# Kernel optimization log

Hardware: AMD Instinct MI355X
Metric: run time of the kernel (lower is better)

The kernel has to match this reference:

```python
import jax, jax.numpy as jnp
import numpy as np
import math

GOLDEN_CENTER = 1.0 / math.e
GOLDEN_LOWER = 0.5 - math.log(4.0 / 3.0)
GOLDEN_UPPER = 0.5

B, T, D = 4, 2048, 1024
E = 8
I = 4096 // (E // 2)  # expert_inter = 1024


def setup_inputs() -> dict:
    key = jax.random.key(0)
    k = jax.random.split(key, 6)
    s_d = 1.0 / math.sqrt(D)
    s_i = 1.0 / math.sqrt(I)
    return {
        "x": jax.random.normal(k[0], (B, T, D), jnp.float32),
        "Wg": jax.random.normal(k[1], (E, D, I), jnp.float32) * s_d,
        "Wu": jax.random.normal(k[2], (E, D, I), jnp.float32) * s_d,
        "Wd": jax.random.normal(k[3], (E, I, D), jnp.float32) * s_i,
        "Wr": jax.random.normal(k[4], (D, E), jnp.float32) * s_d,
        "temperature": jnp.ones((1,), jnp.float32),
    }


def _routing_weights(x, Wr, temperature):
    # inhibition: [B,T,E]
    inh = jax.nn.sigmoid((x @ Wr) / temperature)
    in_zone = (inh >= GOLDEN_LOWER) & (inh <= GOLDEN_UPPER)
    dist = jnp.abs(inh - GOLDEN_CENTER)
    w = jnp.exp(-dist / 0.1) * in_zone.astype(x.dtype)
    wsum = w.sum(axis=-1, keepdims=True)
    no_expert = wsum < 1e-8
    # fallback: softer decay, keep top-2 experts, renormalize
    fb = jnp.exp(-dist / 0.3)
    _, top2 = jax.lax.top_k(fb, 2)  # [B,T,2]
    fb_mask = jax.nn.one_hot(top2, E, dtype=x.dtype).sum(axis=-2)  # [B,T,E]
    fb_w = fb * fb_mask
    fb_w = fb_w / jnp.clip(fb_w.sum(axis=-1, keepdims=True), 1e-8)
    w = jnp.where(no_expert, fb_w, w)
    wsum = w.sum(axis=-1, keepdims=True)
    return w / jnp.clip(wsum, 1e-8)


def reference(x, Wg, Wu, Wd, Wr, temperature):
    weights = _routing_weights(x, Wr, temperature)  # [B,T,E]
    gate = jnp.einsum("btd,edi->beti", x, Wg)
    up = jnp.einsum("btd,edi->beti", x, Wu)
    h = jax.nn.silu(gate) * up  # [B,E,T,I]
    e_out = jnp.einsum("beti,eid->betd", h, Wd)
    out = jnp.einsum("bte,betd->btd", weights, e_out)
    return out
```

## Files before the change

kernel.cpp:

```cpp
#include <hip/hip_runtime.h>
#include <hip/hip_bf16.h>
#include <cstdint>

typedef __attribute__((ext_vector_type(8))) _Float16 f16x8;
typedef __attribute__((ext_vector_type(4))) _Float16 f16x4;
typedef __attribute__((ext_vector_type(4))) float f32x4;

#define GOLDEN_CENTER_F 0.36787944117144233f
#define GOLDEN_LOWER_F  0.21231792754821915f
#define GOLDEN_UPPER_F  0.5f

static constexpr int Dm = 1024;
static constexpr int Im = 1024;
static constexpr int NTOK = 8192;
static constexpr int NE = 8;

__device__ __forceinline__ void async16(const _Float16* g, _Float16* l) {
  __builtin_amdgcn_global_load_lds(
      (const __attribute__((address_space(1))) void*)g,
      (__attribute__((address_space(3))) void*)l,
      16, 0, 0);
}

__global__ void routing_kernel(const float* __restrict__ x, const float* __restrict__ Wr,
                               const float* __restrict__ temp, float* __restrict__ wts) {
  const int wave = threadIdx.x >> 6, lane = threadIdx.x & 63;
  const int t = blockIdx.x * 4 + wave;
  const float* xr = x + (size_t)t * Dm;
  float acc[NE] = {0.f,0.f,0.f,0.f,0.f,0.f,0.f,0.f};
  for (int d = lane; d < Dm; d += 64) {
    float xv = xr[d];
    const float* wr = Wr + (size_t)d * NE;
#pragma unroll
    for (int e = 0; e < NE; ++e) acc[e] += xv * wr[e];
  }
#pragma unroll
  for (int off = 32; off > 0; off >>= 1) {
#pragma unroll
    for (int e = 0; e < NE; ++e) acc[e] += __shfl_down(acc[e], off, 64);
  }
  if (lane == 0) {
    float T = temp[0];
    float w[NE], dist[NE];
    float wsum = 0.f;
#pragma unroll
    for (int e = 0; e < NE; ++e) {
      float inh = 1.f / (1.f + expf(-acc[e] / T));
      dist[e] = fabsf(inh - GOLDEN_CENTER_F);
      bool zone = (inh >= GOLDEN_LOWER_F) && (inh <= GOLDEN_UPPER_F);
      w[e] = zone ? expf(-dist[e] / 0.1f) : 0.f;
      wsum += w[e];
    }
    if (wsum < 1e-8f) {
      float fb[NE];
#pragma unroll
      for (int e = 0; e < NE; ++e) fb[e] = expf(-dist[e] / 0.3f);
      int i1 = 0;
      for (int e = 1; e < NE; ++e) if (fb[e] > fb[i1]) i1 = e;
      int i2 = (i1 == 0) ? 1 : 0;
      for (int e = 0; e < NE; ++e) if (e != i1 && fb[e] > fb[i2]) i2 = e;
      float s = fmaxf(fb[i1] + fb[i2], 1e-8f);
#pragma unroll
      for (int e = 0; e < NE; ++e) w[e] = 0.f;
      w[i1] = fb[i1] / s;
      w[i2] = fb[i2] / s;
      wsum = w[i1] + w[i2];
    }
    float inv = 1.f / fmaxf(wsum, 1e-8f);
#pragma unroll
    for (int e = 0; e < NE; ++e) wts[(size_t)t * NE + e] = w[e] * inv;
  }
}

__global__ void compact_kernel(const float* __restrict__ wts, int* __restrict__ tok,
                               float* __restrict__ wc, int* __restrict__ cnt,
                               int* __restrict__ pos) {
  const int e = blockIdx.x;
  const int tid = threadIdx.x;
  const int wave = tid >> 6, lane = tid & 63;
  __shared__ int wcnt[4];
  __shared__ int s_running;
  if (tid == 0) s_running = 0;
  __syncthreads();
  for (int base = 0; base < NTOK; base += 256) {
    int t = base + tid;
    float w = wts[(size_t)t * NE + e];
    bool act = w > 0.f;
    unsigned long long mask = __ballot(act);
    int prefix = __popcll(mask & ((1ull << lane) - 1ull));
    if (lane == 0) wcnt[wave] = __popcll(mask);
    __syncthreads();
    int wbase = 0;
    for (int i = 0; i < wave; ++i) wbase += wcnt[i];
    int run = s_running;
    int p = run + wbase + prefix;
    pos[(size_t)t * NE + e] = act ? p : -1;
    if (act) {
      tok[(size_t)e * NTOK + p] = t;
      wc[(size_t)e * NTOK + p] = w;
    }
    __syncthreads();
    if (tid == 0) s_running = run + wcnt[0] + wcnt[1] + wcnt[2] + wcnt[3];
    __syncthreads();
  }
  int c = s_running;
  if (tid == 0) cnt[e] = c;
  int padded = (c + 127) & ~127;
  for (int p = c + tid; p < padded; p += 256) {
    tok[(size_t)e * NTOK + p] = 0;
    wc[(size_t)e * NTOK + p] = 0.f;
  }
}

__global__ void cvt_x_kernel(const float* __restrict__ x, _Float16* __restrict__ xb) {
  size_t i = ((size_t)blockIdx.x * 256 + threadIdx.x) * 4;
  float4 v = *(const float4*)(x + i);
  f16x4 o = {(_Float16)v.x, (_Float16)v.y, (_Float16)v.z, (_Float16)v.w};
  *(f16x4*)(xb + i) = o;
}

__global__ void transpose_cvt_kernel(const float* __restrict__ Wg, const float* __restrict__ Wu,
                                     const float* __restrict__ Wd, _Float16* __restrict__ WgT,
                                     _Float16* __restrict__ WuT, _Float16* __restrict__ WdT) {
  __shared__ float tile[32][33];
  const int which = blockIdx.z >> 3;
  const int e = blockIdx.z & 7;
  const float* src = which == 0 ? Wg : which == 1 ? Wu : Wd;
  _Float16* dst = which == 0 ? WgT : which == 1 ? WuT : WdT;
  const size_t base = (size_t)e * 1024 * 1024;
  const int r0 = blockIdx.y * 32, c0 = blockIdx.x * 32;
  const int tx = threadIdx.x & 31, ty = threadIdx.x >> 5;
#pragma unroll
  for (int j = 0; j < 32; j += 8)
    tile[ty + j][tx] = src[base + (size_t)(r0 + ty + j) * 1024 + c0 + tx];
  __syncthreads();
#pragma unroll
  for (int j = 0; j < 32; j += 8)
    dst[base + (size_t)(c0 + ty + j) * 1024 + r0 + tx] = (_Float16)tile[tx][ty + j];
}

__global__ __launch_bounds__(256, 2) void gemm1_kernel(
    const _Float16* __restrict__ A, const _Float16* __restrict__ BgAll,
    const _Float16* __restrict__ BuAll, const int* __restrict__ tok,
    const int* __restrict__ cnt, _Float16* __restrict__ hbuf, int ebase) {
  constexpr int K = Dm;
  const int z = blockIdx.z;
  const int e = ebase + z;
  const int r0 = blockIdx.y * 128;
  if (r0 >= cnt[e]) return;
  const int n0 = blockIdx.x * 128;
  const _Float16* Bg = BgAll + (size_t)e * Dm * Im;
  const _Float16* Bu = BuAll + (size_t)e * Dm * Im;
  _Float16* H = hbuf + (size_t)z * NTOK * Im;
  const int* tk = tok + (size_t)e * NTOK;

  __shared__ _Float16 As[128 * 32];
  __shared__ _Float16 Bgs[128 * 32];
  __shared__ _Float16 Bus[128 * 32];
  const int tid = threadIdx.x;
  const int wave = tid >> 6, lane = tid & 63;
  const int m_off = (wave & 1) * 64, n_off = (wave >> 1) * 64;

  f32x4 accg[4][4], accu[4][4];
#pragma unroll
  for (int i = 0; i < 4; ++i)
#pragma unroll
    for (int j = 0; j < 4; ++j) { accg[i][j] = (f32x4)0.f; accu[i][j] = (f32x4)0.f; }

  const int srow = lane >> 2;
  const int scol = (lane & 3) * 8;
  const int ridx = r0 + wave * 32 + srow;
  const int tA0 = tk[ridx];
  const int tA1 = tk[ridx + 16];
  const _Float16* gA0 = A + (size_t)tA0 * K + scol;
  const _Float16* gA1 = A + (size_t)tA1 * K + scol;
  const _Float16* gBg = Bg + (size_t)(n0 + wave * 32 + srow) * K + scol;
  const _Float16* gBu = Bu + (size_t)(n0 + wave * 32 + srow) * K + scol;
  _Float16* lA  = As  + (wave * 32) * 32;
  _Float16* lBg = Bgs + (wave * 32) * 32;
  _Float16* lBu = Bus + (wave * 32) * 32;

  const int fr = lane & 15, fq = lane >> 4;
  const int aoff = (m_off + fr) * 32 + fq * 8;
  const int boff = (n_off + fr) * 32 + fq * 8;

  for (int k0 = 0; k0 < K; k0 += 32) {
    __syncthreads();
    async16(gA0 + k0, lA);
    async16(gA1 + k0, lA + 16 * 32);
    async16(gBg + k0, lBg);
    async16(gBg + k0 + 16 * K, lBg + 16 * 32);
    async16(gBu + k0, lBu);
    async16(gBu + k0 + 16 * K, lBu + 16 * 32);
    __syncthreads();

    f16x8 af[4], bgf[4], buf2[4];
#pragma unroll
    for (int i = 0; i < 4; ++i) {
      af[i]   = *(const f16x8*)(As  + aoff + i * 16 * 32);
      bgf[i]  = *(const f16x8*)(Bgs + boff + i * 16 * 32);
      buf2[i] = *(const f16x8*)(Bus + boff + i * 16 * 32);
    }
#pragma unroll
    for (int im = 0; im < 4; ++im)
#pragma unroll
      for (int in2 = 0; in2 < 4; ++in2) {
        accg[im][in2] = __builtin_amdgcn_mfma_f32_16x16x32_f16(af[im], bgf[in2], accg[im][in2], 0, 0, 0);
        accu[im][in2] = __builtin_amdgcn_mfma_f32_16x16x32_f16(af[im], buf2[in2], accu[im][in2], 0, 0, 0);
      }
  }

#pragma unroll
  for (int im = 0; im < 4; ++im)
#pragma unroll
    for (int in2 = 0; in2 < 4; ++in2)
#pragma unroll
      for (int r = 0; r < 4; ++r) {
        int row = r0 + m_off + im * 16 + fq * 4 + r;
        int c = n0 + n_off + in2 * 16 + fr;
        float g = accg[im][in2][r], u = accu[im][in2][r];
        float s = g / (1.f + __expf(-g));
        H[(size_t)row * Im + c] = (_Float16)(s * u);
      }
}

__global__ __launch_bounds__(256, 2) void gemm2_kernel(
    const _Float16* __restrict__ hbuf, const _Float16* __restrict__ BAll,
    const int* __restrict__ cnt, _Float16* __restrict__ ebuf, int ebase) {
  constexpr int K = Im;
  const int z = blockIdx.z;
  const int e = ebase + z;
  const int r0 = blockIdx.y * 128;
  if (r0 >= cnt[e]) return;
  const int n0 = blockIdx.x * 128;
  const _Float16* A = hbuf + (size_t)z * NTOK * Im;
  const _Float16* B = BAll + (size_t)e * Im * Dm;
  _Float16* Ez = ebuf + (size_t)z * NTOK * Dm;

  __shared__ _Float16 As[128 * 32];
  __shared__ _Float16 Bs[128 * 32];
  const int tid = threadIdx.x;
  const int wave = tid >> 6, lane = tid & 63;
  const int m_off = (wave & 1) * 64, n_off = (wave >> 1) * 64;

  f32x4 acc[4][4];
#pragma unroll
  for (int i = 0; i < 4; ++i)
#pragma unroll
    for (int j = 0; j < 4; ++j) acc[i][j] = (f32x4)0.f;

  const int srow = lane >> 2;
  const int scol = (lane & 3) * 8;
  const _Float16* gA = A + (size_t)(r0 + wave * 32 + srow) * K + scol;
  const _Float16* gB = B + (size_t)(n0 + wave * 32 + srow) * K + scol;
  _Float16* lA = As + (wave * 32) * 32;
  _Float16* lB = Bs + (wave * 32) * 32;

  const int fr = lane & 15, fq = lane >> 4;
  const int aoff = (m_off + fr) * 32 + fq * 8;
  const int boff = (n_off + fr) * 32 + fq * 8;

  for (int k0 = 0; k0 < K; k0 += 32) {
    __syncthreads();
    async16(gA + k0, lA);
    async16(gA + k0 + 16 * K, lA + 16 * 32);
    async16(gB + k0, lB);
    async16(gB + k0 + 16 * K, lB + 16 * 32);
    __syncthreads();

    f16x8 af[4], bf[4];
#pragma unroll
    for (int i = 0; i < 4; ++i) {
      af[i] = *(const f16x8*)(As + aoff + i * 16 * 32);
      bf[i] = *(const f16x8*)(Bs + boff + i * 16 * 32);
    }
#pragma unroll
    for (int im = 0; im < 4; ++im)
#pragma unroll
      for (int in2 = 0; in2 < 4; ++in2)
        acc[im][in2] = __builtin_amdgcn_mfma_f32_16x16x32_f16(af[im], bf[in2], acc[im][in2], 0, 0, 0);
  }

#pragma unroll
  for (int im = 0; im < 4; ++im)
#pragma unroll
    for (int in2 = 0; in2 < 4; ++in2)
#pragma unroll
      for (int r = 0; r < 4; ++r) {
        int row = m_off + im * 16 + fq * 4 + r;
        int c = n0 + n_off + in2 * 16 + fr;
        Ez[((size_t)(r0 + row)) * Dm + c] = (_Float16)acc[im][in2][r];
      }
}

__global__ void combine_kernel(const _Float16* __restrict__ ebuf, const int* __restrict__ pos,
                               const float* __restrict__ wts, float* __restrict__ out,
                               int ebase, int g, int accum) {
  const int t = blockIdx.x;
  __shared__ int sp[NE];
  __shared__ float sw[NE];
  if (threadIdx.x < g) {
    sp[threadIdx.x] = pos[(size_t)t * NE + ebase + threadIdx.x];
    sw[threadIdx.x] = wts[(size_t)t * NE + ebase + threadIdx.x];
  }
  __syncthreads();
  const int c = threadIdx.x * 4;
  float4 s;
  if (accum) s = *(const float4*)(out + (size_t)t * Dm + c);
  else s = float4{0.f, 0.f, 0.f, 0.f};
  for (int j = 0; j < g; ++j) {
    int p = sp[j];
    if (p >= 0) {
      float w = sw[j];
      f16x4 v = *(const f16x4*)(ebuf + ((size_t)j * NTOK + p) * Dm + c);
      s.x += w * (float)v[0];
      s.y += w * (float)v[1];
      s.z += w * (float)v[2];
      s.w += w * (float)v[3];
    }
  }
  *(float4*)(out + (size_t)t * Dm + c) = s;
}

extern "C" void kernel_launch(void* const* d_in, const int* in_sizes, int n_in,
                              void* d_out, int out_size, void* d_ws, size_t ws_size,
                              hipStream_t stream) {
  const float* x    = (const float*)d_in[0];
  const float* Wg   = (const float*)d_in[1];
  const float* Wu   = (const float*)d_in[2];
  const float* Wd   = (const float*)d_in[3];
  const float* Wr   = (const float*)d_in[4];
  const float* temp = (const float*)d_in[5];
  float* out = (float*)d_out;

  char* ws = (char*)d_ws;
  size_t off = 0;
  auto carve = [&](size_t bytes) {
    char* p = ws + off;
    off = (off + bytes + 255) & ~(size_t)255;
    return p;
  };
  float* wts = (float*)carve((size_t)NTOK * NE * 4);
  int*   tok = (int*)  carve((size_t)NE * NTOK * 4);
  float* wc  = (float*)carve((size_t)NE * NTOK * 4);
  int*   pos = (int*)  carve((size_t)NTOK * NE * 4);
  int*   cnt = (int*)  carve(4096);
  _Float16* xb   = (_Float16*)carve((size_t)NTOK * Dm * 2);
  _Float16* WgT  = (_Float16*)carve((size_t)NE * Dm * Im * 2);
  _Float16* WuT  = (_Float16*)carve((size_t)NE * Dm * Im * 2);
  _Float16* WdT  = (_Float16*)carve((size_t)NE * Dm * Im * 2);
  const size_t fixed_off = off;
  const size_t per_expert = (size_t)NTOK * Im * 2 + (size_t)NTOK * Dm * 2;
  int g = (ws_size >= fixed_off + 8 * per_expert) ? 8 : 4;
  _Float16* hbuf = (_Float16*)carve((size_t)g * NTOK * Im * 2);
  _Float16* ebuf = (_Float16*)carve((size_t)g * NTOK * Dm * 2);

  routing_kernel<<<NTOK / 4, 256, 0, stream>>>(x, Wr, temp, wts);
  compact_kernel<<<NE, 256, 0, stream>>>(wts, tok, wc, cnt, pos);
  cvt_x_kernel<<<(NTOK * Dm) / 1024, 256, 0, stream>>>(x, xb);
  transpose_cvt_kernel<<<dim3(32, 32, 24), 256, 0, stream>>>(Wg, Wu, Wd, WgT, WuT, WdT);

  for (int e0 = 0; e0 < NE; e0 += g) {
    gemm1_kernel<<<dim3(Im / 128, NTOK / 128, g), 256, 0, stream>>>(xb, WgT, WuT, tok, cnt, hbuf, e0);
    gemm2_kernel<<<dim3(Dm / 128, NTOK / 128, g), 256, 0, stream>>>(hbuf, WdT, cnt, ebuf, e0);
    combine_kernel<<<NTOK, 256, 0, stream>>>(ebuf, pos, wts, out, e0, g, e0 > 0);
  }
}
```

Before: 486.7 us.

## Double K-tile to 64 with XOR-swizzled LDS layout in both expert GEMMs

Both expert GEMM kernels now stage a K-slice of 64 instead of 32 per barrier pair, halving the number of __syncthreads rounds. The LDS layout is XOR-swizzled on 16-byte chunks so that the global-to-LDS async loads and the MFMA fragment reads avoid bank conflicts. The launch bounds hint is raised to 3 blocks per CU. LDS use per block doubles, which may limit occupancy for gemm1. The 3-block hint may also force register spills given the large accumulator arrays. Offsets are now 32-bit ints, which remain in range for these sizes.

```diff
diff --git a/kernel.cpp b/kernel.cpp
--- a/kernel.cpp
+++ b/kernel.cpp
@@ -139,7 +139,7 @@
     dst[base + (size_t)(c0 + ty + j) * 1024 + r0 + tx] = (_Float16)tile[tx][ty + j];
 }
 
-__global__ __launch_bounds__(256, 2) void gemm1_kernel(
+__global__ __launch_bounds__(256, 3) void gemm1_kernel(
     const _Float16* __restrict__ A, const _Float16* __restrict__ BgAll,
     const _Float16* __restrict__ BuAll, const int* __restrict__ tok,
     const int* __restrict__ cnt, _Float16* __restrict__ hbuf, int ebase) {
@@ -154,9 +154,9 @@
   _Float16* H = hbuf + (size_t)z * NTOK * Im;
   const int* tk = tok + (size_t)e * NTOK;
 
-  __shared__ _Float16 As[128 * 32];
-  __shared__ _Float16 Bgs[128 * 32];
-  __shared__ _Float16 Bus[128 * 32];
+  __shared__ _Float16 As[128 * 64];
+  __shared__ _Float16 Bgs[128 * 64];
+  __shared__ _Float16 Bus[128 * 64];
   const int tid = threadIdx.x;
   const int wave = tid >> 6, lane = tid & 63;
   const int m_off = (wave & 1) * 64, n_off = (wave >> 1) * 64;
@@ -167,47 +167,55 @@
 #pragma unroll
     for (int j = 0; j < 4; ++j) { accg[i][j] = (f32x4)0.f; accu[i][j] = (f32x4)0.f; }
 
-  const int srow = lane >> 2;
-  const int scol = (lane & 3) * 8;
-  const int ridx = r0 + wave * 32 + srow;
-  const int tA0 = tk[ridx];
-  const int tA1 = tk[ridx + 16];
-  const _Float16* gA0 = A + (size_t)tA0 * K + scol;
-  const _Float16* gA1 = A + (size_t)tA1 * K + scol;
-  const _Float16* gBg = Bg + (size_t)(n0 + wave * 32 + srow) * K + scol;
-  const _Float16* gBu = Bu + (size_t)(n0 + wave * 32 + srow) * K + scol;
-  _Float16* lA  = As  + (wave * 32) * 32;
-  _Float16* lBg = Bgs + (wave * 32) * 32;
-  _Float16* lBu = Bus + (wave * 32) * 32;
+  const int sr = lane >> 3;
+  const int jchunk = (lane & 7) ^ sr;
+  int oA[4], oBg[4], oBu[4];
+#pragma unroll
+  for (int q = 0; q < 4; ++q) {
+    int rloc = wave * 32 + q * 8 + sr;
+    int tA = tk[r0 + rloc];
+    oA[q]  = tA * K + jchunk * 8;
+    oBg[q] = (n0 + rloc) * K + jchunk * 8;
+    oBu[q] = oBg[q];
+  }
+  _Float16* lA  = As  + wave * 32 * 64;
+  _Float16* lBg = Bgs + wave * 32 * 64;
+  _Float16* lBu = Bus + wave * 32 * 64;
 
   const int fr = lane & 15, fq = lane >> 4;
-  const int aoff = (m_off + fr) * 32 + fq * 8;
-  const int boff = (n_off + fr) * 32 + fq * 8;
-
-  for (int k0 = 0; k0 < K; k0 += 32) {
-    __syncthreads();
-    async16(gA0 + k0, lA);
-    async16(gA1 + k0, lA + 16 * 32);
-    async16(gBg + k0, lBg);
-    async16(gBg + k0 + 16 * K, lBg + 16 * 32);
-    async16(gBu + k0, lBu);
-    async16(gBu + k0 + 16 * K, lBu + 16 * 32);
-    __syncthreads();
-
-    f16x8 af[4], bgf[4], buf2[4];
-#pragma unroll
-    for (int i = 0; i < 4; ++i) {
-      af[i]   = *(const f16x8*)(As  + aoff + i * 16 * 32);
-      bgf[i]  = *(const f16x8*)(Bgs + boff + i * 16 * 32);
-      buf2[i] = *(const f16x8*)(Bus + boff + i * 16 * 32);
-    }
-#pragma unroll
-    for (int im = 0; im < 4; ++im)
-#pragma unroll
-      for (int in2 = 0; in2 < 4; ++in2) {
-        accg[im][in2] = __builtin_amdgcn_mfma_f32_16x16x32_f16(af[im], bgf[in2], accg[im][in2], 0, 0, 0);
-        accu[im][in2] = __builtin_amdgcn_mfma_f32_16x16x32_f16(af[im], buf2[in2], accu[im][in2], 0, 0, 0);
+  const int x0 = fq ^ (fr & 7);
+  const int aoff = (m_off + fr) * 64;
+  const int boff = (n_off + fr) * 64;
+  const int c0 = x0 * 8, c1 = (x0 ^ 4) * 8;
+
+  for (int k0 = 0; k0 < K; k0 += 64) {
+    __syncthreads();
+#pragma unroll
+    for (int q = 0; q < 4; ++q) async16(A + oA[q] + k0, lA + q * 512);
+#pragma unroll
+    for (int q = 0; q < 4; ++q) async16(Bg + oBg[q] + k0, lBg + q * 512);
+#pragma unroll
+    for (int q = 0; q < 4; ++q) async16(Bu + oBu[q] + k0, lBu + q * 512);
+    __syncthreads();
+
+#pragma unroll
+    for (int ks = 0; ks < 2; ++ks) {
+      const int co = ks ? c1 : c0;
+      f16x8 af[4], bgf[4], buf2[4];
+#pragma unroll
+      for (int i = 0; i < 4; ++i) {
+        af[i]   = *(const f16x8*)(As  + aoff + i * 1024 + co);
+        bgf[i]  = *(const f16x8*)(Bgs + boff + i * 1024 + co);
+        buf2[i] = *(const f16x8*)(Bus + boff + i * 1024 + co);
       }
+#pragma unroll
+      for (int im = 0; im < 4; ++im)
+#pragma unroll
+        for (int in2 = 0; in2 < 4; ++in2) {
+          accg[im][in2] = __builtin_amdgcn_mfma_f32_16x16x32_f16(af[im], bgf[in2], accg[im][in2], 0, 0, 0);
+          accu[im][in2] = __builtin_amdgcn_mfma_f32_16x16x32_f16(af[im], buf2[in2], accu[im][in2], 0, 0, 0);
+        }
+    }
   }
 
 #pragma unroll
@@ -224,7 +232,7 @@
       }
 }
 
-__global__ __launch_bounds__(256, 2) void gemm2_kernel(
+__global__ __launch_bounds__(256, 3) void gemm2_kernel(
     const _Float16* __restrict__ hbuf, const _Float16* __restrict__ BAll,
     const int* __restrict__ cnt, _Float16* __restrict__ ebuf, int ebase) {
   constexpr int K = Im;
@@ -237,8 +245,8 @@
   const _Float16* B = BAll + (size_t)e * Im * Dm;
   _Float16* Ez = ebuf + (size_t)z * NTOK * Dm;
 
-  __shared__ _Float16 As[128 * 32];
-  __shared__ _Float16 Bs[128 * 32];
+  __shared__ _Float16 As[128 * 64];
+  __shared__ _Float16 Bs[128 * 64];
   const int tid = threadIdx.x;
   const int wave = tid >> 6, lane = tid & 63;
   const int m_off = (wave & 1) * 64, n_off = (wave >> 1) * 64;
@@ -249,36 +257,47 @@
 #pragma unroll
     for (int j = 0; j < 4; ++j) acc[i][j] = (f32x4)0.f;
 
-  const int srow = lane >> 2;
-  const int scol = (lane & 3) * 8;
-  const _Float16* gA = A + (size_t)(r0 + wave * 32 + srow) * K + scol;
-  const _Float16* gB = B + (size_t)(n0 + wave * 32 + srow) * K + scol;
-  _Float16* lA = As + (wave * 32) * 32;
-  _Float16* lB = Bs + (wave * 32) * 32;
+  const int sr = lane >> 3;
+  const int jchunk = (lane & 7) ^ sr;
+  int oA[4], oB[4];
+#pragma unroll
+  for (int q = 0; q < 4; ++q) {
+    int rloc = wave * 32 + q * 8 + sr;
+    oA[q] = (r0 + rloc) * K + jchunk * 8;
+    oB[q] = (n0 + rloc) * K + jchunk * 8;
+  }
+  _Float16* lA = As + wave * 32 * 64;
+  _Float16* lB = Bs + wave * 32 * 64;
 
   const int fr = lane & 15, fq = lane >> 4;
-  const int aoff = (m_off + fr) * 32 + fq * 8;
-  const int boff = (n_off + fr) * 32 + fq * 8;
-
-  for (int k0 = 0; k0 < K; k0 += 32) {
-    __syncthreads();
-    async16(gA + k0, lA);
-    async16(gA + k0 + 16 * K, lA + 16 * 32);
-    async16(gB + k0, lB);
-    async16(gB + k0 + 16 * K, lB + 16 * 32);
-    __syncthreads();
-
-    f16x8 af[4], bf[4];
-#pragma unroll
-    for (int i = 0; i < 4; ++i) {
-      af[i] = *(const f16x8*)(As + aoff + i * 16 * 32);
-      bf[i] = *(const f16x8*)(Bs + boff + i * 16 * 32);
-    }
-#pragma unroll
-    for (int im = 0; im < 4; ++im)
-#pragma unroll
-      for (int in2 = 0; in2 < 4; ++in2)
-        acc[im][in2] = __builtin_amdgcn_mfma_f32_16x16x32_f16(af[im], bf[in2], acc[im][in2], 0, 0, 0);
+  const int x0 = fq ^ (fr & 7);
+  const int aoff = (m_off + fr) * 64;
+  const int boff = (n_off + fr) * 64;
+  const int c0 = x0 * 8, c1 = (x0 ^ 4) * 8;
+
+  for (int k0 = 0; k0 < K; k0 += 64) {
+    __syncthreads();
+#pragma unroll
+    for (int q = 0; q < 4; ++q) async16(A + oA[q] + k0, lA + q * 512);
+#pragma unroll
+    for (int q = 0; q < 4; ++q) async16(B + oB[q] + k0, lB + q * 512);
+    __syncthreads();
+
+#pragma unroll
+    for (int ks = 0; ks < 2; ++ks) {
+      const int co = ks ? c1 : c0;
+      f16x8 af[4], bf[4];
+#pragma unroll
+      for (int i = 0; i < 4; ++i) {
+        af[i] = *(const f16x8*)(As + aoff + i * 1024 + co);
+        bf[i] = *(const f16x8*)(Bs + boff + i * 1024 + co);
+      }
+#pragma unroll
+      for (int im = 0; im < 4; ++im)
+#pragma unroll
+        for (int in2 = 0; in2 < 4; ++in2)
+          acc[im][in2] = __builtin_amdgcn_mfma_f32_16x16x32_f16(af[im], bf[in2], acc[im][in2], 0, 0, 0);
+    }
   }
 
 #pragma unroll
```

Measured after the change: 846.4 us. 73.9% more time.
